# Kernel tuning notes

Hardware: AMD Instinct MI355X
Metric: run time of the kernel (lower is better)

The kernel has to match this reference:

```python
import jax, jax.numpy as jnp
import numpy as np

N, E, F, D, L, G, T = 100000, 600000, 64, 128, 3, 256, 10
BN_EPS = 1e-5


def _bn(x, g, b):
    # training-mode BatchNorm1d over all rows (biased variance)
    m = x.mean(0)
    v = jnp.mean((x - m) ** 2, 0)
    return (x - m) * jax.lax.rsqrt(v + BN_EPS) * g + b


def _masked_bn(x, mask, g, b):
    # BatchNorm1d computed only over rows where mask==1 (target nodes),
    # matching torch's nn(s[target_nodes_id]) which normalizes the subset.
    cnt = jnp.maximum(mask.sum(), 1.0)
    m = (mask[:, None] * x).sum(0) / cnt
    v = (mask[:, None] * (x - m) ** 2).sum(0) / cnt
    return (x - m) * jax.lax.rsqrt(v + BN_EPS) * g + b


def setup_inputs() -> dict:
    key = jax.random.key(0)
    ks = jax.random.split(key, 32)
    inp = {}
    inp["dag_x"] = jax.random.normal(ks[0], (N, F), dtype=jnp.float32)
    inp["dag_edge_index"] = jax.random.randint(ks[1], (2, E), 0, N)
    inp["edge_multiplicities"] = jax.random.uniform(ks[2], (E,), dtype=jnp.float32)
    inp["dag_layers_mask"] = jax.random.randint(ks[3], (E,), 0, L)
    inp["batch"] = jnp.sort(jax.random.randint(ks[4], (N,), 0, G))
    inp["leaves0"] = jax.random.randint(ks[5], (50000,), 0, N)
    inp["readouts"] = jax.random.randint(ks[6], (L + 1, 20000), 0, N)
    # node_features_transformation params
    inp["W1"] = jax.random.normal(ks[7], (F, D), dtype=jnp.float32) / np.sqrt(F)
    inp["b1"] = jnp.zeros((D,), jnp.float32)
    inp["g1"] = jnp.ones((D,), jnp.float32)
    inp["be1"] = jnp.zeros((D,), jnp.float32)
    inp["W2"] = jax.random.normal(ks[8], (D, D), dtype=jnp.float32) / np.sqrt(D)
    inp["b2"] = jnp.zeros((D,), jnp.float32)
    inp["g2"] = jnp.ones((D,), jnp.float32)
    inp["be2"] = jnp.zeros((D,), jnp.float32)
    # per-DAG-layer MLP params (stacked over L layers)
    inp["dag_W1"] = jax.random.normal(ks[9], (L, D, D), dtype=jnp.float32) / np.sqrt(D)
    inp["dag_b1"] = jnp.zeros((L, D), jnp.float32)
    inp["dag_g1"] = jnp.ones((L, D), jnp.float32)
    inp["dag_be1"] = jnp.zeros((L, D), jnp.float32)
    inp["dag_W2"] = jax.random.normal(ks[10], (L, D, D), dtype=jnp.float32) / np.sqrt(D)
    inp["dag_b2"] = jnp.zeros((L, D), jnp.float32)
    inp["dag_g2"] = jnp.ones((L, D), jnp.float32)
    inp["dag_be2"] = jnp.zeros((L, D), jnp.float32)
    inp["dag_eps"] = jnp.zeros((L,), jnp.float32)
    # readout linear (last_layer)
    inp["Wl"] = jax.random.normal(ks[11], (D, T), dtype=jnp.float32) / np.sqrt(D)
    inp["bl"] = jnp.zeros((T,), jnp.float32)
    return inp


def reference(dag_x, edge_multiplicities, W1, b1, g1, be1, W2, b2, g2, be2,
              dag_W1, dag_b1, dag_g1, dag_be1, dag_W2, dag_b2, dag_g2, dag_be2,
              dag_eps, Wl, bl, dag_edge_index, dag_layers_mask, batch, leaves0,
              readouts):
    # node feature transformation: Linear-BN-ReLU x2
    feature = jax.nn.relu(_bn(dag_x @ W1 + b1, g1, be1))
    feature = jax.nn.relu(_bn(feature @ W2 + b2, g2, be2))
    # x starts as zeros except on layer-0 leaves
    x = jnp.zeros_like(feature).at[leaves0].set(feature[leaves0])
    src, dst = dag_edge_index[0], dag_edge_index[1]
    for i in range(L):
        active = (dag_layers_mask == i)
        w = jnp.where(active, edge_multiplicities, 0.0)  # [E]
        # weighted gather-scatter message passing (inactive edges contribute 0)
        E_X = jax.ops.segment_sum(x[src] * w[:, None], dst, num_segments=N)
        tcnt = jax.ops.segment_sum(active.astype(jnp.float32), dst, num_segments=N)
        is_t = (tcnt > 0).astype(x.dtype)  # [N] target-node mask
        # self-loop term (1+eps)*feature only on targets, plus aggregated messages
        s = is_t[:, None] * ((1.0 + dag_eps[i]) * feature) + E_X
        h = jax.nn.relu(_masked_bn(s @ dag_W1[i] + dag_b1[i], is_t, dag_g1[i], dag_be1[i]))
        h = jax.nn.relu(_masked_bn(h @ dag_W2[i] + dag_b2[i], is_t, dag_g2[i], dag_be2[i]))
        # MLP applied only on target nodes, then residual add of x
        x = jnp.where(is_t[:, None] > 0, h, s) + x
    # multi-height readout: sum-pool per graph at each height, then mean over heights
    pooled = []
    for i in range(L + 1):
        idx = readouts[i]
        pooled.append(jax.ops.segment_sum(x[idx], batch[idx], num_segments=G))
    out = jnp.stack(pooled, 1).mean(1) @ Wl + bl  # [G, T]
    return out
```

## Files before the change

### kernel.cpp

```cpp
#include <hip/hip_runtime.h>

constexpr int Nn = 100000;
constexpr int Ee = 600000;
constexpr int Dd = 128;
constexpr int Ll = 3;
constexpr int Gg = 256;
constexpr int Tt = 10;
constexpr float BN_EPS = 1e-5f;
constexpr int NREP = 16;
constexpr int PSL = 8;
constexpr int PR = 32;

typedef __attribute__((ext_vector_type(8))) short short8v;
typedef __attribute__((ext_vector_type(4))) float f32x4;

__device__ inline ushort bf_hi(float f) {
  unsigned u = __float_as_uint(f);
  unsigned r = (u + 0x7FFFu + ((u >> 16) & 1u)) >> 16;
  return (ushort)r;
}
__device__ inline float bf_f(ushort h) {
  return __uint_as_float(((unsigned)h) << 16);
}

__device__ inline void compute_ss_lds(const float* __restrict__ stats,
                                      const float* __restrict__ g,
                                      const float* __restrict__ be, float cnt,
                                      float* ssS) {
  const int c = threadIdx.x;
  if (c < 128) {
    float S = 0.f, Q = 0.f;
#pragma unroll
    for (int r = 0; r < NREP; ++r) {
      S += stats[r * 512 + c];
      Q += stats[r * 512 + 256 + c];
    }
    const float m = S / cnt;
    const float v = Q / cnt - m * m;
    const float sc = g[c] * rsqrtf(v + BN_EPS);
    ssS[c] = sc;
    ssS[128 + c] = be[c] - m * sc;
  }
}

template <bool NORM_A, bool MASKED>
__global__ __launch_bounds__(256, 4) void gemm_bf16(
    const ushort* __restrict__ A, const ushort* __restrict__ WTh,
    const ushort* __restrict__ WTl, const float* __restrict__ bias,
    const float* __restrict__ statsIn, const float* __restrict__ gN,
    const float* __restrict__ beN, const float* __restrict__ cntPtr,
    const int* __restrict__ tmask, ushort* __restrict__ C,
    float* __restrict__ statsOut, int nrows) {
  __shared__ ushort SB[16384];
  __shared__ float ssS[256];
  ushort* Bh = SB;
  ushort* Bl = SB + 8192;
  const int tid = threadIdx.x;
  const int w = tid >> 6, lane = tid & 63, lr = lane & 15, lg = lane >> 4;
  const int rt = blockIdx.x >> 1, ct = blockIdx.x & 1;
  const int rowBase = rt * 128, cBase = ct * 64;
  const int rep = blockIdx.x & (NREP - 1);

  {
    const int cc = tid >> 2;
    const ushort* sH = WTh + (size_t)(cBase + cc) * 128;
    const ushort* sL = WTl + (size_t)(cBase + cc) * 128;
    char* BhB = (char*)Bh;
    char* BlB = (char*)Bl;
#pragma unroll
    for (int i = 0; i < 4; ++i) {
      const int slot = (tid & 3) * 4 + i;
      const int off = (cc * 256 + slot * 16) ^ ((cc & 7) << 4);
      *(short8v*)(BhB + off) = *(const short8v*)(sH + slot * 8);
      *(short8v*)(BlB + off) = *(const short8v*)(sL + slot * 8);
    }
  }
  if (NORM_A) {
    const float cnt = cntPtr ? fmaxf(cntPtr[0], 1.f) : (float)nrows;
    compute_ss_lds(statsIn, gN, beN, cnt, ssS);
  }

  const int row0 = rowBase + w * 32 + lr;
  const int row1 = row0 + 16;
  const bool ok0 = row0 < nrows, ok1 = row1 < nrows;
  const short8v szero = {0, 0, 0, 0, 0, 0, 0, 0};
  const ushort* aP0 = A + (size_t)row0 * 128 + lg * 8;
  const ushort* aP1 = A + (size_t)row1 * 128 + lg * 8;
  short8v ar0[4], ar1[4];
#pragma unroll
  for (int c = 0; c < 4; ++c) {
    ar0[c] = ok0 ? *(const short8v*)(aP0 + c * 32) : szero;
    ar1[c] = ok1 ? *(const short8v*)(aP1 + c * 32) : szero;
  }
  __syncthreads();

  const f32x4 fzero = {0.f, 0.f, 0.f, 0.f};
  f32x4 acc[2][4];
#pragma unroll
  for (int i = 0; i < 2; ++i)
#pragma unroll
    for (int j = 0; j < 4; ++j) acc[i][j] = fzero;

  const char* BhB = (const char*)Bh;
  const char* BlB = (const char*)Bl;
  __builtin_amdgcn_s_setprio(1);
#pragma unroll
  for (int c = 0; c < 4; ++c) {
    short8v a0 = ar0[c], a1 = ar1[c];
    if (NORM_A) {
      const int kb = c * 32 + lg * 8;
      const float4 s0 = *(const float4*)&ssS[kb];
      const float4 s1 = *(const float4*)&ssS[kb + 4];
      const float4 h0 = *(const float4*)&ssS[128 + kb];
      const float4 h1 = *(const float4*)&ssS[128 + kb + 4];
      const float sv[8] = {s0.x, s0.y, s0.z, s0.w, s1.x, s1.y, s1.z, s1.w};
      const float hv[8] = {h0.x, h0.y, h0.z, h0.w, h1.x, h1.y, h1.z, h1.w};
#pragma unroll
      for (int j = 0; j < 8; ++j) {
        a0[j] = (short)bf_hi(fmaxf(fmaf(bf_f((ushort)a0[j]), sv[j], hv[j]), 0.f));
        a1[j] = (short)bf_hi(fmaxf(fmaf(bf_f((ushort)a1[j]), sv[j], hv[j]), 0.f));
      }
    }
#pragma unroll
    for (int nf = 0; nf < 4; ++nf) {
      const int brow = nf * 16 + lr;
      const int off = (brow * 256 + (c * 4 + lg) * 16) ^ ((lr & 7) << 4);
      const short8v bh = *(const short8v*)(BhB + off);
      const short8v bl = *(const short8v*)(BlB + off);
      acc[0][nf] = __builtin_amdgcn_mfma_f32_16x16x32_bf16(a0, bh, acc[0][nf], 0, 0, 0);
      acc[1][nf] = __builtin_amdgcn_mfma_f32_16x16x32_bf16(a1, bh, acc[1][nf], 0, 0, 0);
      acc[0][nf] = __builtin_amdgcn_mfma_f32_16x16x32_bf16(a0, bl, acc[0][nf], 0, 0, 0);
      acc[1][nf] = __builtin_amdgcn_mfma_f32_16x16x32_bf16(a1, bl, acc[1][nf], 0, 0, 0);
    }
  }
  __builtin_amdgcn_s_setprio(0);

  float mrow[2][4];
#pragma unroll
  for (int mf = 0; mf < 2; ++mf)
#pragma unroll
    for (int rr = 0; rr < 4; ++rr) {
      const int row = rowBase + w * 32 + mf * 16 + lg * 4 + rr;
      float m = 0.f;
      if (row < nrows) m = MASKED ? ((tmask[row] > 0) ? 1.f : 0.f) : 1.f;
      mrow[mf][rr] = m;
    }
  __syncthreads();
  ushort* Cs = SB;
  float* Sred = (float*)(SB + 9216);
  float* Sq = Sred + 256;
#pragma unroll
  for (int nf = 0; nf < 4; ++nf) {
    const int col = nf * 16 + lr;
    const float bcol = bias[cBase + col];
    float ps = 0.f, pq = 0.f;
#pragma unroll
    for (int mf = 0; mf < 2; ++mf) {
      const f32x4 vv = acc[mf][nf];
#pragma unroll
      for (int rr = 0; rr < 4; ++rr) {
        const float o = vv[rr] + bcol;
        const int rl = w * 32 + mf * 16 + lg * 4 + rr;
        Cs[rl * 72 + col] = bf_hi(o);
        const float mo = mrow[mf][rr] * o;
        ps += mo;
        pq += mo * o;
      }
    }
    ps += __shfl_xor(ps, 16);
    ps += __shfl_xor(ps, 32);
    pq += __shfl_xor(pq, 16);
    pq += __shfl_xor(pq, 32);
    if (lg == 0) {
      Sred[w * 64 + col] = ps;
      Sq[w * 64 + col] = pq;
    }
  }
  __syncthreads();
  {
    const int rl = tid >> 1, half = tid & 1;
    const int grow = rowBase + rl;
    if (grow < nrows) {
      ushort* dstp = C + (size_t)grow * 128 + cBase + half * 32;
      const ushort* srcp = Cs + rl * 72 + half * 32;
#pragma unroll
      for (int j = 0; j < 4; ++j)
        *(short8v*)(dstp + j * 8) = *(const short8v*)(srcp + j * 8);
    }
  }
  if (tid < 64) {
    float s = 0.f;
#pragma unroll
    for (int q = 0; q < 4; ++q) s += Sred[q * 64 + tid];
    atomicAdd(&statsOut[rep * 512 + cBase + tid], s);
  } else if (tid < 128) {
    float s = 0.f;
#pragma unroll
    for (int q = 0; q < 4; ++q) s += Sq[q * 64 + tid - 64];
    atomicAdd(&statsOut[rep * 512 + 256 + cBase + tid - 64], s);
  }
}

__global__ __launch_bounds__(256, 4) void gemm_agg(
    const ushort* __restrict__ x, const ushort* __restrict__ feat,
    const int* __restrict__ offs, const int2* __restrict__ pairs,
    const float* __restrict__ deps, int layer, const ushort* __restrict__ WTh,
    const ushort* __restrict__ WTl, const float* __restrict__ bias,
    ushort* __restrict__ C, float* __restrict__ statsOut,
    int* __restrict__ tmask, int nrows) {
  __shared__ ushort SB[16384];
  ushort* Bh = SB;
  ushort* Bl = SB + 8192;
  const int tid = threadIdx.x;
  const int w = tid >> 6, lane = tid & 63, lr = lane & 15, lg = lane >> 4;
  const int rt = blockIdx.x >> 1, ct = blockIdx.x & 1;
  const int rowBase = rt * 128, cBase = ct * 64;
  const int rep = blockIdx.x & (NREP - 1);

  {
    const int cc = tid >> 2;
    const ushort* sH = WTh + (size_t)(cBase + cc) * 128;
    const ushort* sL = WTl + (size_t)(cBase + cc) * 128;
    char* BhB = (char*)Bh;
    char* BlB = (char*)Bl;
#pragma unroll
    for (int i = 0; i < 4; ++i) {
      const int slot = (tid & 3) * 4 + i;
      const int off = (cc * 256 + slot * 16) ^ ((cc & 7) << 4);
      *(short8v*)(BhB + off) = *(const short8v*)(sH + slot * 8);
      *(short8v*)(BlB + off) = *(const short8v*)(sL + slot * 8);
    }
  }

  const float ce = 1.f + deps[layer];
  const int row0 = rowBase + w * 32 + lr;
  const int row1 = row0 + 16;
  int o0a = 0, o1a = 0, o0b = 0, o1b = 0;
  if (row0 < nrows) {
    o0a = offs[layer * Nn + row0];
    o1a = offs[layer * Nn + row0 + 1];
  }
  if (row1 < nrows) {
    o0b = offs[layer * Nn + row1];
    o1b = offs[layer * Nn + row1 + 1];
  }
  if (lg == 0) {
    if (row0 < nrows) tmask[row0] = (o1a > o0a) ? 1 : 0;
    if (row1 < nrows) tmask[row1] = (o1b > o0b) ? 1 : 0;
  }

  short8v ar0[4], ar1[4];
  {
    float a[4][8];
#pragma unroll
    for (int c = 0; c < 4; ++c)
#pragma unroll
      for (int j = 0; j < 8; ++j) a[c][j] = 0.f;
    for (int p = o0a; p < o1a; ++p) {
      const int2 pr = pairs[p];
      const float wgt = __int_as_float(pr.y);
      const ushort* xr = x + (size_t)pr.x * 128 + lg * 8;
#pragma unroll
      for (int c = 0; c < 4; ++c) {
        const short8v xv = *(const short8v*)(xr + c * 32);
#pragma unroll
        for (int j = 0; j < 8; ++j)
          a[c][j] = fmaf(wgt, bf_f((ushort)xv[j]), a[c][j]);
      }
    }
    if (o1a > o0a) {
      const ushort* fr = feat + (size_t)row0 * 128 + lg * 8;
#pragma unroll
      for (int c = 0; c < 4; ++c) {
        const short8v fv = *(const short8v*)(fr + c * 32);
#pragma unroll
        for (int j = 0; j < 8; ++j)
          a[c][j] = fmaf(ce, bf_f((ushort)fv[j]), a[c][j]);
      }
    }
#pragma unroll
    for (int c = 0; c < 4; ++c)
#pragma unroll
      for (int j = 0; j < 8; ++j) ar0[c][j] = (short)bf_hi(a[c][j]);
  }
  {
    float a[4][8];
#pragma unroll
    for (int c = 0; c < 4; ++c)
#pragma unroll
      for (int j = 0; j < 8; ++j) a[c][j] = 0.f;
    for (int p = o0b; p < o1b; ++p) {
      const int2 pr = pairs[p];
      const float wgt = __int_as_float(pr.y);
      const ushort* xr = x + (size_t)pr.x * 128 + lg * 8;
#pragma unroll
      for (int c = 0; c < 4; ++c) {
        const short8v xv = *(const short8v*)(xr + c * 32);
#pragma unroll
        for (int j = 0; j < 8; ++j)
          a[c][j] = fmaf(wgt, bf_f((ushort)xv[j]), a[c][j]);
      }
    }
    if (o1b > o0b) {
      const ushort* fr = feat + (size_t)row1 * 128 + lg * 8;
#pragma unroll
      for (int c = 0; c < 4; ++c) {
        const short8v fv = *(const short8v*)(fr + c * 32);
#pragma unroll
        for (int j = 0; j < 8; ++j)
          a[c][j] = fmaf(ce, bf_f((ushort)fv[j]), a[c][j]);
      }
    }
#pragma unroll
    for (int c = 0; c < 4; ++c)
#pragma unroll
      for (int j = 0; j < 8; ++j) ar1[c][j] = (short)bf_hi(a[c][j]);
  }
  __syncthreads();

  const f32x4 fzero = {0.f, 0.f, 0.f, 0.f};
  f32x4 acc[2][4];
#pragma unroll
  for (int i = 0; i < 2; ++i)
#pragma unroll
    for (int j = 0; j < 4; ++j) acc[i][j] = fzero;

  const char* BhB = (const char*)Bh;
  const char* BlB = (const char*)Bl;
  __builtin_amdgcn_s_setprio(1);
#pragma unroll
  for (int c = 0; c < 4; ++c) {
    const short8v a0 = ar0[c], a1 = ar1[c];
#pragma unroll
    for (int nf = 0; nf < 4; ++nf) {
      const int brow = nf * 16 + lr;
      const int off = (brow * 256 + (c * 4 + lg) * 16) ^ ((lr & 7) << 4);
      const short8v bh = *(const short8v*)(BhB + off);
      const short8v bl = *(const short8v*)(BlB + off);
      acc[0][nf] = __builtin_amdgcn_mfma_f32_16x16x32_bf16(a0, bh, acc[0][nf], 0, 0, 0);
      acc[1][nf] = __builtin_amdgcn_mfma_f32_16x16x32_bf16(a1, bh, acc[1][nf], 0, 0, 0);
      acc[0][nf] = __builtin_amdgcn_mfma_f32_16x16x32_bf16(a0, bl, acc[0][nf], 0, 0, 0);
      acc[1][nf] = __builtin_amdgcn_mfma_f32_16x16x32_bf16(a1, bl, acc[1][nf], 0, 0, 0);
    }
  }
  __builtin_amdgcn_s_setprio(0);

  const float dga = (o1a > o0a) ? 1.f : 0.f;
  const float dgb = (o1b > o0b) ? 1.f : 0.f;
  float mrow[2][4];
#pragma unroll
  for (int rr = 0; rr < 4; ++rr) {
    const int srcl = lg * 4 + rr;
    mrow[0][rr] = __shfl(dga, (w << 6 & 0) + srcl, 64);
    mrow[1][rr] = __shfl(dgb, srcl, 64);
  }
#pragma unroll
  for (int mf = 0; mf < 2; ++mf)
#pragma unroll
    for (int rr = 0; rr < 4; ++rr) {
      const int row = rowBase + w * 32 + mf * 16 + lg * 4 + rr;
      if (row >= nrows) mrow[mf][rr] = 0.f;
    }
  __syncthreads();
  ushort* Cs = SB;
  float* Sred = (float*)(SB + 9216);
  float* Sq = Sred + 256;
#pragma unroll
  for (int nf = 0; nf < 4; ++nf) {
    const int col = nf * 16 + lr;
    const float bcol = bias[cBase + col];
    float ps = 0.f, pq = 0.f;
#pragma unroll
    for (int mf = 0; mf < 2; ++mf) {
      const f32x4 vv = acc[mf][nf];
#pragma unroll
      for (int rr = 0; rr < 4; ++rr) {
        const float o = vv[rr] + bcol;
        const int rl = w * 32 + mf * 16 + lg * 4 + rr;
        Cs[rl * 72 + col] = bf_hi(o);
        const float mo = mrow[mf][rr] * o;
        ps += mo;
        pq += mo * o;
      }
    }
    ps += __shfl_xor(ps, 16);
    ps += __shfl_xor(ps, 32);
    pq += __shfl_xor(pq, 16);
    pq += __shfl_xor(pq, 32);
    if (lg == 0) {
      Sred[w * 64 + col] = ps;
      Sq[w * 64 + col] = pq;
    }
  }
  __syncthreads();
  {
    const int rl = tid >> 1, half = tid & 1;
    const int grow = rowBase + rl;
    if (grow < nrows) {
      ushort* dstp = C + (size_t)grow * 128 + cBase + half * 32;
      const ushort* srcp = Cs + rl * 72 + half * 32;
#pragma unroll
      for (int j = 0; j < 4; ++j)
        *(short8v*)(dstp + j * 8) = *(const short8v*)(srcp + j * 8);
    }
  }
  if (tid < 64) {
    float s = 0.f;
#pragma unroll
    for (int q = 0; q < 4; ++q) s += Sred[q * 64 + tid];
    atomicAdd(&statsOut[rep * 512 + cBase + tid], s);
  } else if (tid < 128) {
    float s = 0.f;
#pragma unroll
    for (int q = 0; q < 4; ++q) s += Sq[q * 64 + tid - 64];
    atomicAdd(&statsOut[rep * 512 + 256 + cBase + tid - 64], s);
  }
}

__global__ __launch_bounds__(256, 4) void gemm_f32a(
    const float* __restrict__ A, const ushort* __restrict__ WTh,
    const ushort* __restrict__ WTl, const float* __restrict__ bias,
    ushort* __restrict__ C, float* __restrict__ statsOut, int nrows) {
  __shared__ ushort SB[11264];
  ushort* Bh = SB;
  ushort* Bl = SB + 4096;
  const int tid = threadIdx.x;
  const int w = tid >> 6, lane = tid & 63, lr = lane & 15, lg = lane >> 4;
  const int rt = blockIdx.x >> 1, ct = blockIdx.x & 1;
  const int rowBase = rt * 128, cBase = ct * 64;
  const int rep = blockIdx.x & (NREP - 1);

  {
    const int cc = tid >> 2;
    const ushort* sH = WTh + (size_t)(cBase + cc) * 64;
    const ushort* sL = WTl + (size_t)(cBase + cc) * 64;
    char* BhB = (char*)Bh;
    char* BlB = (char*)Bl;
#pragma unroll
    for (int i = 0; i < 2; ++i) {
      const int slot = (tid & 3) * 2 + i;
      const int off = (cc * 128 + slot * 16) ^ ((cc & 7) << 4);
      *(short8v*)(BhB + off) = *(const short8v*)(sH + slot * 8);
      *(short8v*)(BlB + off) = *(const short8v*)(sL + slot * 8);
    }
  }

  const int row0 = rowBase + w * 32 + lr;
  const int row1 = row0 + 16;
  const bool ok0 = row0 < nrows, ok1 = row1 < nrows;
  const float4 fz4 = make_float4(0.f, 0.f, 0.f, 0.f);
  const float* aP0 = A + (size_t)row0 * 64 + lg * 8;
  const float* aP1 = A + (size_t)row1 * 64 + lg * 8;
  float4 ar0[2][2], ar1[2][2];
#pragma unroll
  for (int c = 0; c < 2; ++c) {
    ar0[c][0] = ok0 ? *(const float4*)(aP0 + c * 32) : fz4;
    ar0[c][1] = ok0 ? *(const float4*)(aP0 + c * 32 + 4) : fz4;
    ar1[c][0] = ok1 ? *(const float4*)(aP1 + c * 32) : fz4;
    ar1[c][1] = ok1 ? *(const float4*)(aP1 + c * 32 + 4) : fz4;
  }
  __syncthreads();

  const f32x4 fzero = {0.f, 0.f, 0.f, 0.f};
  f32x4 acc[2][4];
#pragma unroll
  for (int i = 0; i < 2; ++i)
#pragma unroll
    for (int j = 0; j < 4; ++j) acc[i][j] = fzero;

  const char* BhB = (const char*)Bh;
  const char* BlB = (const char*)Bl;
  __builtin_amdgcn_s_setprio(1);
#pragma unroll
  for (int c = 0; c < 2; ++c) {
    const float v0[8] = {ar0[c][0].x, ar0[c][0].y, ar0[c][0].z, ar0[c][0].w,
                         ar0[c][1].x, ar0[c][1].y, ar0[c][1].z, ar0[c][1].w};
    const float v1[8] = {ar1[c][0].x, ar1[c][0].y, ar1[c][0].z, ar1[c][0].w,
                         ar1[c][1].x, ar1[c][1].y, ar1[c][1].z, ar1[c][1].w};
    short8v a0h, a0l, a1h, a1l;
#pragma unroll
    for (int j = 0; j < 8; ++j) {
      ushort hh = bf_hi(v0[j]);
      a0h[j] = (short)hh;
      a0l[j] = (short)bf_hi(v0[j] - bf_f(hh));
      hh = bf_hi(v1[j]);
      a1h[j] = (short)hh;
      a1l[j] = (short)bf_hi(v1[j] - bf_f(hh));
    }
#pragma unroll
    for (int nf = 0; nf < 4; ++nf) {
      const int brow = nf * 16 + lr;
      const int off = (brow * 128 + (c * 4 + lg) * 16) ^ ((lr & 7) << 4);
      const short8v bh = *(const short8v*)(BhB + off);
      const short8v bl = *(const short8v*)(BlB + off);
      acc[0][nf] = __builtin_amdgcn_mfma_f32_16x16x32_bf16(a0h, bh, acc[0][nf], 0, 0, 0);
      acc[1][nf] = __builtin_amdgcn_mfma_f32_16x16x32_bf16(a1h, bh, acc[1][nf], 0, 0, 0);
      acc[0][nf] = __builtin_amdgcn_mfma_f32_16x16x32_bf16(a0l, bh, acc[0][nf], 0, 0, 0);
      acc[1][nf] = __builtin_amdgcn_mfma_f32_16x16x32_bf16(a1l, bh, acc[1][nf], 0, 0, 0);
      acc[0][nf] = __builtin_amdgcn_mfma_f32_16x16x32_bf16(a0h, bl, acc[0][nf], 0, 0, 0);
      acc[1][nf] = __builtin_amdgcn_mfma_f32_16x16x32_bf16(a1h, bl, acc[1][nf], 0, 0, 0);
    }
  }
  __builtin_amdgcn_s_setprio(0);

  __syncthreads();
  ushort* Cs = SB;
  float* Sred = (float*)(SB + 9216);
  float* Sq = Sred + 256;
#pragma unroll
  for (int nf = 0; nf < 4; ++nf) {
    const int col = nf * 16 + lr;
    const float bcol = bias[cBase + col];
    float ps = 0.f, pq = 0.f;
#pragma unroll
    for (int mf = 0; mf < 2; ++mf) {
      const f32x4 vv = acc[mf][nf];
#pragma unroll
      for (int rr = 0; rr < 4; ++rr) {
        const float o = vv[rr] + bcol;
        const int rl = w * 32 + mf * 16 + lg * 4 + rr;
        Cs[rl * 72 + col] = bf_hi(o);
        const int row = rowBase + rl;
        const float m = (row < nrows) ? 1.f : 0.f;
        const float mo = m * o;
        ps += mo;
        pq += mo * o;
      }
    }
    ps += __shfl_xor(ps, 16);
    ps += __shfl_xor(ps, 32);
    pq += __shfl_xor(pq, 16);
    pq += __shfl_xor(pq, 32);
    if (lg == 0) {
      Sred[w * 64 + col] = ps;
      Sq[w * 64 + col] = pq;
    }
  }
  __syncthreads();
  {
    const int rl = tid >> 1, half = tid & 1;
    const int grow = rowBase + rl;
    if (grow < nrows) {
      ushort* dstp = C + (size_t)grow * 128 + cBase + half * 32;
      const ushort* srcp = Cs + rl * 72 + half * 32;
#pragma unroll
      for (int j = 0; j < 4; ++j)
        *(short8v*)(dstp + j * 8) = *(const short8v*)(srcp + j * 8);
    }
  }
  if (tid < 64) {
    float s = 0.f;
#pragma unroll
    for (int q = 0; q < 4; ++q) s += Sred[q * 64 + tid];
    atomicAdd(&statsOut[rep * 512 + cBase + tid], s);
  } else if (tid < 128) {
    float s = 0.f;
#pragma unroll
    for (int q = 0; q < 4; ++q) s += Sq[q * 64 + tid - 64];
    atomicAdd(&statsOut[rep * 512 + 256 + cBase + tid - 64], s);
  }
}

__global__ __launch_bounds__(256) void wsplit_kernel(
    const float* __restrict__ W1, const float* __restrict__ W2,
    const float* __restrict__ dW1, const float* __restrict__ dW2,
    ushort* __restrict__ wsT) {
  const int t = blockIdx.x * 256 + threadIdx.x;
  const int slot = t >> 14;
  const int idx = t & 16383;
  if (slot >= 8) return;
  const int Ks = (slot == 0) ? 64 : 128;
  if (idx >= 128 * Ks) return;
  const int c = idx / Ks;
  const int k = idx - c * Ks;
  float v;
  if (slot == 0) v = W1[k * 128 + c];
  else if (slot == 1) v = W2[k * 128 + c];
  else if (slot < 5) v = dW1[(slot - 2) * 16384 + k * 128 + c];
  else v = dW2[(slot - 5) * 16384 + k * 128 + c];
  const ushort h = bf_hi(v);
  const ushort l = bf_hi(v - bf_f(h));
  wsT[slot * 32768 + c * Ks + k] = h;
  wsT[slot * 32768 + 16384 + c * Ks + k] = l;
}

__global__ __launch_bounds__(256) void normrelu_kernel(
    const ushort* __restrict__ in, const float* __restrict__ stats,
    const float* __restrict__ g, const float* __restrict__ be, float cntFixed,
    ushort* __restrict__ outp, ushort* __restrict__ xz) {
  __shared__ float ssS[256];
  compute_ss_lds(stats, g, be, cntFixed, ssS);
  __syncthreads();
  const int tid = threadIdx.x;
  const int c4 = (tid & 31) * 4;
  const float4 sc = *(const float4*)&ssS[c4];
  const float4 sh = *(const float4*)&ssS[128 + c4];
  const int rowBase = blockIdx.x * 64;
  const ushort4 z4 = make_ushort4(0, 0, 0, 0);
#pragma unroll
  for (int it = 0; it < 8; ++it) {
    const int row = rowBase + it * 8 + (tid >> 5);
    if (row >= Nn) continue;
    const size_t idx = (size_t)row * 32 + (tid & 31);
    const ushort4 v = ((const ushort4*)in)[idx];
    ushort4 o;
    o.x = bf_hi(fmaxf(fmaf(bf_f(v.x), sc.x, sh.x), 0.f));
    o.y = bf_hi(fmaxf(fmaf(bf_f(v.y), sc.y, sh.y), 0.f));
    o.z = bf_hi(fmaxf(fmaf(bf_f(v.z), sc.z, sh.z), 0.f));
    o.w = bf_hi(fmaxf(fmaf(bf_f(v.w), sc.w, sh.w), 0.f));
    ((ushort4*)outp)[idx] = o;
    ((ushort4*)xz)[idx] = z4;
  }
}

__global__ __launch_bounds__(256) void normrelu_acc_kernel(
    const ushort* __restrict__ in, const float* __restrict__ stats,
    const float* __restrict__ g, const float* __restrict__ be,
    const float* __restrict__ cntPtr, const int* __restrict__ tmask,
    ushort* __restrict__ x) {
  __shared__ float ssS[256];
  compute_ss_lds(stats, g, be, fmaxf(cntPtr[0], 1.f), ssS);
  __syncthreads();
  const int tid = threadIdx.x;
  const int c4 = (tid & 31) * 4;
  const float4 sc = *(const float4*)&ssS[c4];
  const float4 sh = *(const float4*)&ssS[128 + c4];
  const int rowBase = blockIdx.x * 64;
#pragma unroll
  for (int it = 0; it < 8; ++it) {
    const int row = rowBase + it * 8 + (tid >> 5);
    if (row >= Nn || tmask[row] <= 0) continue;
    const size_t idx = (size_t)row * 32 + (tid & 31);
    const ushort4 v = ((const ushort4*)in)[idx];
    ushort4 xo = ((const ushort4*)x)[idx];
    xo.x = bf_hi(bf_f(xo.x) + fmaxf(fmaf(bf_f(v.x), sc.x, sh.x), 0.f));
    xo.y = bf_hi(bf_f(xo.y) + fmaxf(fmaf(bf_f(v.y), sc.y, sh.y), 0.f));
    xo.z = bf_hi(bf_f(xo.z) + fmaxf(fmaf(bf_f(v.z), sc.z, sh.z), 0.f));
    xo.w = bf_hi(bf_f(xo.w) + fmaxf(fmaf(bf_f(v.w), sc.w, sh.w), 0.f));
    ((ushort4*)x)[idx] = xo;
  }
}

__global__ __launch_bounds__(256) void scatter_leaves_kernel(
    const int* __restrict__ leaves, const ushort* __restrict__ feat,
    ushort* __restrict__ x, int nl) {
  const int gid = blockIdx.x * 256 + threadIdx.x;
  const int j = gid >> 5;
  if (j >= nl) return;
  const int node = leaves[j];
  const int c4 = (gid & 31) * 4;
  *(ushort4*)&x[(size_t)node * 128 + c4] =
      *(const ushort4*)&feat[(size_t)node * 128 + c4];
}

__global__ __launch_bounds__(256) void deg_count_kernel(
    const int* __restrict__ dst, const int* __restrict__ lmask,
    int* __restrict__ cnts) {
  const int e = blockIdx.x * 256 + threadIdx.x;
  if (e >= Ee) return;
  atomicAdd(&cnts[lmask[e] * Nn + dst[e]], 1);
}

__global__ __launch_bounds__(256) void scan1_kernel(const int* __restrict__ in,
                                                    int* __restrict__ out,
                                                    int* __restrict__ bsum,
                                                    float* __restrict__ tcountf,
                                                    int n) {
  __shared__ int lds[256];
  __shared__ float tcS[3];
  const int tid = threadIdx.x;
  const int base = blockIdx.x * 2048 + tid * 8;
  int vals[8];
  int tsum = 0;
  float t0 = 0.f, t1 = 0.f, t2 = 0.f;
#pragma unroll
  for (int j = 0; j < 8; ++j) {
    const int i = base + j;
    const int v = (i < n) ? in[i] : 0;
    if (v > 0) {
      if (i < Nn) t0 += 1.f;
      else if (i < 2 * Nn) t1 += 1.f;
      else t2 += 1.f;
    }
    vals[j] = tsum;
    tsum += v;
  }
  lds[tid] = tsum;
  if (tid < 3) tcS[tid] = 0.f;
  __syncthreads();
  if (t0 != 0.f) atomicAdd(&tcS[0], t0);
  if (t1 != 0.f) atomicAdd(&tcS[1], t1);
  if (t2 != 0.f) atomicAdd(&tcS[2], t2);
  for (int off = 1; off < 256; off <<= 1) {
    const int y = (tid >= off) ? lds[tid - off] : 0;
    __syncthreads();
    lds[tid] += y;
    __syncthreads();
  }
  const int texcl = (tid > 0) ? lds[tid - 1] : 0;
#pragma unroll
  for (int j = 0; j < 8; ++j)
    if (base + j < n) out[base + j] = texcl + vals[j];
  if (tid == 255) bsum[blockIdx.x] = lds[255];
  __syncthreads();
  if (tid < 3 && tcS[tid] != 0.f) atomicAdd(&tcountf[tid], tcS[tid]);
}

__global__ __launch_bounds__(256) void scan3_kernel(int* __restrict__ out,
                                                    int* __restrict__ cursor,
                                                    const int* __restrict__ bsum,
                                                    int nb, int n, int etot) {
  __shared__ int bs[256];
  const int tid = threadIdx.x;
  const int v = (tid < nb) ? bsum[tid] : 0;
  bs[tid] = v;
  __syncthreads();
  for (int off = 1; off < 256; off <<= 1) {
    const int y = (tid >= off) ? bs[tid - off] : 0;
    __syncthreads();
    bs[tid] += y;
    __syncthreads();
  }
  const int i = blockIdx.x * 256 + tid;
  if (i >= n) return;
  const int b = i >> 11;
  const int excl = (b > 0) ? bs[b - 1] : 0;
  const int val = out[i] + excl;
  out[i] = val;
  cursor[i] = val;
  if (i == n - 1) out[n] = etot;
}

__global__ __launch_bounds__(256) void csr_fill_kernel(
    const int* __restrict__ src, const int* __restrict__ dst,
    const float* __restrict__ mult, const int* __restrict__ lmask,
    int* __restrict__ cursor, int2* __restrict__ pairs) {
  const int e = blockIdx.x * 256 + threadIdx.x;
  if (e >= Ee) return;
  const int slot = atomicAdd(&cursor[lmask[e] * Nn + dst[e]], 1);
  pairs[slot] = make_int2(src[e], __float_as_int(mult[e]));
}

__global__ __launch_bounds__(256) void phist_kernel(const int* __restrict__ ridx,
                                                    const int* __restrict__ batch,
                                                    int* __restrict__ cnt, int n) {
  const int i = blockIdx.x * 256 + threadIdx.x;
  if (i >= n) return;
  atomicAdd(&cnt[batch[ridx[i]] * PR + (i & (PR - 1))], 1);
}

__global__ void pscan_kernel(int* __restrict__ cnt, int* __restrict__ cur) {
  __shared__ int l[256];
  const int t = threadIdx.x;
  const int base = t * 32;
  int vals[32];
  int tsum = 0;
#pragma unroll
  for (int j = 0; j < 32; ++j) {
    const int v = cnt[base + j];
    vals[j] = tsum;
    tsum += v;
  }
  l[t] = tsum;
  __syncthreads();
  for (int off = 1; off < 256; off <<= 1) {
    const int y = (t >= off) ? l[t - off] : 0;
    __syncthreads();
    l[t] += y;
    __syncthreads();
  }
  const int excl = (t > 0) ? l[t - 1] : 0;
#pragma unroll
  for (int j = 0; j < 32; ++j) {
    const int v = excl + vals[j];
    cnt[base + j] = v;
    cur[base + j] = v;
  }
}

__global__ __launch_bounds__(256) void pfill_kernel(const int* __restrict__ ridx,
                                                    const int* __restrict__ batch,
                                                    int* __restrict__ cur,
                                                    int* __restrict__ sorted,
                                                    int n) {
  const int i = blockIdx.x * 256 + threadIdx.x;
  if (i >= n) return;
  const int node = ridx[i];
  const int slot = atomicAdd(&cur[batch[node] * PR + (i & (PR - 1))], 1);
  sorted[slot] = node;
}

__global__ __launch_bounds__(256) void ppool_kernel(const int* __restrict__ sorted,
                                                    const int* __restrict__ offs,
                                                    const ushort* __restrict__ x,
                                                    float* __restrict__ Ppart,
                                                    int n) {
  __shared__ float part[4][256];
  const int bid = blockIdx.x;
  const int g = bid >> 3, slice = bid & (PSL - 1);
  const int w = threadIdx.x >> 6;
  const int lane = threadIdx.x & 63;
  const int o0 = offs[g * PR];
  const int o1 = (g < Gg - 1) ? offs[(g + 1) * PR] : n;
  float ax = 0.f, ay = 0.f;
  for (int p = o0 + slice * 4 + w; p < o1; p += 32) {
    const int node = sorted[p];
    const ushort2 xv = *(const ushort2*)&x[(size_t)node * 128 + lane * 2];
    ax += bf_f(xv.x);
    ay += bf_f(xv.y);
  }
  part[w][lane * 2] = ax;
  part[w][lane * 2 + 1] = ay;
  __syncthreads();
  if (threadIdx.x < 128) {
    const int c = threadIdx.x;
    Ppart[(size_t)bid * 128 + c] =
        part[0][c] + part[1][c] + part[2][c] + part[3][c];
  }
}

__global__ __launch_bounds__(128) void pout_kernel(
    const float* __restrict__ Ppart, const float* __restrict__ Wl,
    const float* __restrict__ bl, float* __restrict__ out) {
  __shared__ float Pl[128];
  const int g = blockIdx.x;
  const int t = threadIdx.x;
  float s = 0.f;
#pragma unroll
  for (int r = 0; r < PSL; ++r) s += Ppart[(size_t)(g * PSL + r) * 128 + t];
  Pl[t] = s * 0.25f;
  __syncthreads();
  if (t < Tt) {
    float acc = 0.f;
    for (int c = 0; c < 128; ++c) acc += Pl[c] * Wl[c * Tt + t];
    out[g * Tt + t] = acc + bl[t];
  }
}

extern "C" void kernel_launch(void* const* d_in, const int* in_sizes, int n_in,
                              void* d_out, int out_size, void* d_ws,
                              size_t ws_size, hipStream_t stream) {
  const float* dag_x = (const float*)d_in[0];
  const int* eidx = (const int*)d_in[1];
  const int* src = eidx;
  const int* dst = eidx + Ee;
  const float* mult = (const float*)d_in[2];
  const int* lmask = (const int*)d_in[3];
  const int* batch = (const int*)d_in[4];
  const int* leaves = (const int*)d_in[5];
  const int* readouts = (const int*)d_in[6];
  const float* W1 = (const float*)d_in[7];
  const float* b1 = (const float*)d_in[8];
  const float* g1 = (const float*)d_in[9];
  const float* be1 = (const float*)d_in[10];
  const float* W2 = (const float*)d_in[11];
  const float* b2 = (const float*)d_in[12];
  const float* g2 = (const float*)d_in[13];
  const float* be2 = (const float*)d_in[14];
  const float* dW1 = (const float*)d_in[15];
  const float* db1 = (const float*)d_in[16];
  const float* dg1 = (const float*)d_in[17];
  const float* dbe1 = (const float*)d_in[18];
  const float* dW2 = (const float*)d_in[19];
  const float* db2 = (const float*)d_in[20];
  const float* dg2 = (const float*)d_in[21];
  const float* dbe2 = (const float*)d_in[22];
  const float* deps = (const float*)d_in[23];
  const float* Wl = (const float*)d_in[24];
  const float* bl = (const float*)d_in[25];
  float* out = (float*)d_out;

  const size_t ND = (size_t)Nn * Dd;
  ushort* feat = (ushort*)d_ws;
  ushort* xbuf = feat + ND;
  ushort* Abuf = xbuf + ND;
  ushort* Bbuf = Abuf + ND;
  float* statsAll = (float*)(Bbuf + ND);
  float* tcountf = statsAll + 8 * 8192;
  int* tmask = (int*)(tcountf + 8);
  ushort* wsT = (ushort*)(tmask + Nn);
  int* offs = (int*)(wsT + 262144);
  int2* pairs = (int2*)(offs + 3 * Nn + 4);

  int* cnts = (int*)xbuf;
  int* cursor = cnts + 3 * Nn;
  int* bsum = cursor + 3 * Nn;
  const int nridx = in_sizes[6];
  const int nleaves = in_sizes[5];
  int* pcnt = (int*)Abuf;
  int* pcur = pcnt + Gg * PR;
  int* sorted = pcur + Gg * PR;
  float* Ppart = (float*)(sorted + nridx);

  dim3 blk(256);
  hipMemsetAsync(statsAll, 0, (8 * 8192 + 8) * sizeof(float), stream);
  wsplit_kernel<<<512, blk, 0, stream>>>(W1, W2, dW1, dW2, wsT);

  hipMemsetAsync(cnts, 0, 3 * Nn * sizeof(int), stream);
  deg_count_kernel<<<2344, blk, 0, stream>>>(dst, lmask, cnts);
  scan1_kernel<<<147, blk, 0, stream>>>(cnts, offs, bsum, tcountf, 3 * Nn);
  scan3_kernel<<<1172, blk, 0, stream>>>(offs, cursor, bsum, 147, 3 * Nn, Ee);
  csr_fill_kernel<<<2344, blk, 0, stream>>>(src, dst, mult, lmask, cursor, pairs);

  const int gGemm = 782 * 2;
  gemm_f32a<<<gGemm, blk, 0, stream>>>(dag_x, wsT, wsT + 16384, b1, Abuf,
                                       statsAll + 0 * 8192, Nn);
  gemm_bf16<true, false><<<gGemm, blk, 0, stream>>>(
      Abuf, wsT + 32768, wsT + 32768 + 16384, b2, statsAll + 0 * 8192, g1, be1,
      nullptr, nullptr, Bbuf, statsAll + 1 * 8192, Nn);
  normrelu_kernel<<<1563, blk, 0, stream>>>(Bbuf, statsAll + 1 * 8192, g2, be2,
                                            (float)Nn, feat, xbuf);
  scatter_leaves_kernel<<<6250, blk, 0, stream>>>(leaves, feat, xbuf, nleaves);

  for (int layer = 0; layer < Ll; ++layer) {
    const int so1 = (2 + layer) * 32768;
    const int so2 = (5 + layer) * 32768;
    const int po = layer * Dd;
    float* st1 = statsAll + (size_t)(2 + 2 * layer) * 8192;
    float* st2 = statsAll + (size_t)(3 + 2 * layer) * 8192;
    gemm_agg<<<gGemm, blk, 0, stream>>>(xbuf, feat, offs, pairs, deps, layer,
                                        wsT + so1, wsT + so1 + 16384, db1 + po,
                                        Bbuf, st1, tmask, Nn);
    gemm_bf16<true, true><<<gGemm, blk, 0, stream>>>(
        Bbuf, wsT + so2, wsT + so2 + 16384, db2 + po, st1, dg1 + po, dbe1 + po,
        tcountf + layer, tmask, Abuf, st2, Nn);
    normrelu_acc_kernel<<<1563, blk, 0, stream>>>(
        Abuf, st2, dg2 + po, dbe2 + po, tcountf + layer, tmask, xbuf);
  }

  hipMemsetAsync(pcnt, 0, Gg * PR * sizeof(int), stream);
  const int gIdx = (nridx + 255) / 256;
  phist_kernel<<<gIdx, blk, 0, stream>>>(readouts, batch, pcnt, nridx);
  pscan_kernel<<<1, blk, 0, stream>>>(pcnt, pcur);
  pfill_kernel<<<gIdx, blk, 0, stream>>>(readouts, batch, pcur, sorted, nridx);
  ppool_kernel<<<Gg * PSL, blk, 0, stream>>>(sorted, pcnt, xbuf, Ppart, nridx);
  pout_kernel<<<Gg, dim3(128), 0, stream>>>(Ppart, Wl, bl, out);
}
```

Baseline: 460.7 us.

## Compute full 128-column output per block in gemm_agg to avoid duplicate aggregation

gemm_agg previously split each 128-row tile across two blocks of 64 output columns, so both blocks redid the costly CSR gather-aggregation of the same rows. Now one block covers all 128 columns with the full weight matrix in shared memory and twice as many accumulators, so the aggregation runs once per row. The price is double the LDS (64KB), more registers, launch bounds lowered to 2 blocks per CU, and half as many blocks, which reduces occupancy and latency hiding for the gather.

Result: no change. 460.2 us (-0.1%).

```diff
diff --git a/kernel.cpp b/kernel.cpp
--- a/kernel.cpp
+++ b/kernel.cpp
@@ -201,34 +201,34 @@
   }
 }
 
-__global__ __launch_bounds__(256, 4) void gemm_agg(
+__global__ __launch_bounds__(256, 2) void gemm_agg(
     const ushort* __restrict__ x, const ushort* __restrict__ feat,
     const int* __restrict__ offs, const int2* __restrict__ pairs,
     const float* __restrict__ deps, int layer, const ushort* __restrict__ WTh,
     const ushort* __restrict__ WTl, const float* __restrict__ bias,
     ushort* __restrict__ C, float* __restrict__ statsOut,
     int* __restrict__ tmask, int nrows) {
-  __shared__ ushort SB[16384];
+  __shared__ ushort SB[32768];
   ushort* Bh = SB;
-  ushort* Bl = SB + 8192;
+  ushort* Bl = SB + 16384;
   const int tid = threadIdx.x;
   const int w = tid >> 6, lane = tid & 63, lr = lane & 15, lg = lane >> 4;
-  const int rt = blockIdx.x >> 1, ct = blockIdx.x & 1;
-  const int rowBase = rt * 128, cBase = ct * 64;
+  const int rowBase = blockIdx.x * 128;
   const int rep = blockIdx.x & (NREP - 1);
 
   {
-    const int cc = tid >> 2;
-    const ushort* sH = WTh + (size_t)(cBase + cc) * 128;
-    const ushort* sL = WTl + (size_t)(cBase + cc) * 128;
+    const int cc = tid >> 1;
+    const int half = tid & 1;
+    const ushort* sH = WTh + (size_t)cc * 128 + half * 64;
+    const ushort* sL = WTl + (size_t)cc * 128 + half * 64;
     char* BhB = (char*)Bh;
     char* BlB = (char*)Bl;
 #pragma unroll
-    for (int i = 0; i < 4; ++i) {
-      const int slot = (tid & 3) * 4 + i;
+    for (int i = 0; i < 8; ++i) {
+      const int slot = half * 8 + i;
       const int off = (cc * 256 + slot * 16) ^ ((cc & 7) << 4);
-      *(short8v*)(BhB + off) = *(const short8v*)(sH + slot * 8);
-      *(short8v*)(BlB + off) = *(const short8v*)(sL + slot * 8);
+      *(short8v*)(BhB + off) = *(const short8v*)(sH + i * 8);
+      *(short8v*)(BlB + off) = *(const short8v*)(sL + i * 8);
     }
   }
 
@@ -319,11 +319,11 @@
   __syncthreads();
 
   const f32x4 fzero = {0.f, 0.f, 0.f, 0.f};
-  f32x4 acc[2][4];
+  f32x4 acc[2][8];
 #pragma unroll
   for (int i = 0; i < 2; ++i)
 #pragma unroll
-    for (int j = 0; j < 4; ++j) acc[i][j] = fzero;
+    for (int j = 0; j < 8; ++j) acc[i][j] = fzero;
 
   const char* BhB = (const char*)Bh;
   const char* BlB = (const char*)Bl;
@@ -332,7 +332,7 @@
   for (int c = 0; c < 4; ++c) {
     const short8v a0 = ar0[c], a1 = ar1[c];
 #pragma unroll
-    for (int nf = 0; nf < 4; ++nf) {
+    for (int nf = 0; nf < 8; ++nf) {
       const int brow = nf * 16 + lr;
       const int off = (brow * 256 + (c * 4 + lg) * 16) ^ ((lr & 7) << 4);
       const short8v bh = *(const short8v*)(BhB + off);
@@ -351,7 +351,7 @@
 #pragma unroll
   for (int rr = 0; rr < 4; ++rr) {
     const int srcl = lg * 4 + rr;
-    mrow[0][rr] = __shfl(dga, (w << 6 & 0) + srcl, 64);
+    mrow[0][rr] = __shfl(dga, srcl, 64);
     mrow[1][rr] = __shfl(dgb, srcl, 64);
   }
 #pragma unroll
@@ -363,12 +363,12 @@
     }
   __syncthreads();
   ushort* Cs = SB;
-  float* Sred = (float*)(SB + 9216);
-  float* Sq = Sred + 256;
-#pragma unroll
-  for (int nf = 0; nf < 4; ++nf) {
+  float* Sred = (float*)(SB + 17408);
+  float* Sq = Sred + 512;
+#pragma unroll
+  for (int nf = 0; nf < 8; ++nf) {
     const int col = nf * 16 + lr;
-    const float bcol = bias[cBase + col];
+    const float bcol = bias[col];
     float ps = 0.f, pq = 0.f;
 #pragma unroll
     for (int mf = 0; mf < 2; ++mf) {
@@ -377,7 +377,7 @@
       for (int rr = 0; rr < 4; ++rr) {
         const float o = vv[rr] + bcol;
         const int rl = w * 32 + mf * 16 + lg * 4 + rr;
-        Cs[rl * 72 + col] = bf_hi(o);
+        Cs[rl * 136 + col] = bf_hi(o);
         const float mo = mrow[mf][rr] * o;
         ps += mo;
         pq += mo * o;
@@ -388,8 +388,8 @@
     pq += __shfl_xor(pq, 16);
     pq += __shfl_xor(pq, 32);
     if (lg == 0) {
-      Sred[w * 64 + col] = ps;
-      Sq[w * 64 + col] = pq;
+      Sred[w * 128 + col] = ps;
+      Sq[w * 128 + col] = pq;
     }
   }
   __syncthreads();
@@ -397,23 +397,25 @@
     const int rl = tid >> 1, half = tid & 1;
     const int grow = rowBase + rl;
     if (grow < nrows) {
-      ushort* dstp = C + (size_t)grow * 128 + cBase + half * 32;
-      const ushort* srcp = Cs + rl * 72 + half * 32;
-#pragma unroll
-      for (int j = 0; j < 4; ++j)
+      ushort* dstp = C + (size_t)grow * 128 + half * 64;
+      const ushort* srcp = Cs + rl * 136 + half * 64;
+#pragma unroll
+      for (int j = 0; j < 8; ++j)
         *(short8v*)(dstp + j * 8) = *(const short8v*)(srcp + j * 8);
     }
   }
-  if (tid < 64) {
+  {
+    const int col = tid & 127;
     float s = 0.f;
-#pragma unroll
-    for (int q = 0; q < 4; ++q) s += Sred[q * 64 + tid];
-    atomicAdd(&statsOut[rep * 512 + cBase + tid], s);
-  } else if (tid < 128) {
-    float s = 0.f;
-#pragma unroll
-    for (int q = 0; q < 4; ++q) s += Sq[q * 64 + tid - 64];
-    atomicAdd(&statsOut[rep * 512 + 256 + cBase + tid - 64], s);
+    if (tid < 128) {
+#pragma unroll
+      for (int q = 0; q < 4; ++q) s += Sred[q * 128 + col];
+      atomicAdd(&statsOut[rep * 512 + col], s);
+    } else {
+#pragma unroll
+      for (int q = 0; q < 4; ++q) s += Sq[q * 128 + col];
+      atomicAdd(&statsOut[rep * 512 + 256 + col], s);
+    }
   }
 }
 
@@ -918,9 +920,9 @@
     const int po = layer * Dd;
     float* st1 = statsAll + (size_t)(2 + 2 * layer) * 8192;
     float* st2 = statsAll + (size_t)(3 + 2 * layer) * 8192;
-    gemm_agg<<<gGemm, blk, 0, stream>>>(xbuf, feat, offs, pairs, deps, layer,
-                                        wsT + so1, wsT + so1 + 16384, db1 + po,
-                                        Bbuf, st1, tmask, Nn);
+    gemm_agg<<<782, blk, 0, stream>>>(xbuf, feat, offs, pairs, deps, layer,
+                                      wsT + so1, wsT + so1 + 16384, db1 + po,
+                                      Bbuf, st1, tmask, Nn);
     gemm_bf16<true, true><<<gGemm, blk, 0, stream>>>(
         Bbuf, wsT + so2, wsT + so2 + 16384, db2 + po, st1, dg1 + po, dbe1 + po,
         tcountf + layer, tmask, Abuf, st2, Nn);
```
